# Performance work log

Measured on AMD Instinct MI355X. Metric: run time of the kernel, lower is better.

Reference implementation:

```python
import jax, jax.numpy as jnp
import numpy as np

FMAP = 160        # feature-map side -> N = FMAP*FMAP anchors
STRIDE = 4.0      # anchor grid stride in pixels
ANCHOR_SIZE = 32.0
NUM_CLASSES = 8
MAX_GT = 50
BATCH = 32


def setup_inputs() -> dict:
    key = jax.random.key(0)
    k0, k1, k2, k3, k4, k5 = jax.random.split(key, 6)
    B, C, H = BATCH, NUM_CLASSES, FMAP
    cls_output = jax.random.normal(k0, (B, C, 1, H, H), jnp.float32)
    reg_output = jax.random.normal(k1, (B, 4, 1, H, H), jnp.float32) * 0.3
    # anchor grid: one ANCHOR_SIZE box per feature-map cell; flatten order
    # matches torch's reshape over (H, W)
    c = (jnp.arange(H, dtype=jnp.float32) + 0.5) * STRIDE
    cy, cx = jnp.meshgrid(c, c, indexing='ij')   # row-major [H, W]
    cx = cx.reshape(-1); cy = cy.reshape(-1)
    half = ANCHOR_SIZE / 2.0
    anchors = jnp.stack([cx - half, cy - half, cx + half, cy + half], axis=1)
    # padded GT boxes, all geometrically valid (x1<x2, y1<y2)
    cxy = jax.random.uniform(k2, (B, MAX_GT, 2), jnp.float32, 64.0, 576.0)
    wh = jax.random.uniform(k3, (B, MAX_GT, 2), jnp.float32, 16.0, 128.0)
    gt_boxes = jnp.concatenate([cxy - wh / 2.0, cxy + wh / 2.0], axis=-1)
    gt_labels = jax.random.randint(k4, (B, MAX_GT), 0, NUM_CLASSES)
    num_boxes = jax.random.randint(k5, (B,), 0, MAX_GT + 1)
    return dict(cls_output=cls_output, reg_output=reg_output, anchors=anchors,
                gt_boxes=gt_boxes, gt_labels=gt_labels, num_boxes=num_boxes)


def _decode_boxes(reg, anchors):
    # inverse of the encoding in the loss: tx=(gt_cx-a_cx)*(4/aw) then (tx+1)/2
    aw = anchors[:, 2] - anchors[:, 0]
    ah = anchors[:, 3] - anchors[:, 1]
    acx = anchors[:, 0] + 0.5 * aw
    acy = anchors[:, 1] + 0.5 * ah
    tx = reg[..., 0] * 2.0 - 1.0
    ty = reg[..., 1] * 2.0 - 1.0
    cx = acx + tx * aw / 4.0
    cy = acy + ty * ah / 4.0
    w = aw * jnp.exp(reg[..., 2])
    h = ah * jnp.exp(reg[..., 3])
    return jnp.stack([cx - w / 2, cy - h / 2, cx + w / 2, cy + h / 2], axis=-1)


def _pairwise_iou(b1, b2):
    # b1 [B,N,4], b2 [B,M,4] -> [B,N,M]
    lt = jnp.maximum(b1[:, :, None, :2], b2[:, None, :, :2])
    rb = jnp.minimum(b1[:, :, None, 2:], b2[:, None, :, 2:])
    wh = jnp.clip(rb - lt, 0.0)
    inter = wh[..., 0] * wh[..., 1]
    a1 = (b1[..., 2] - b1[..., 0]) * (b1[..., 3] - b1[..., 1])
    a2 = (b2[..., 2] - b2[..., 0]) * (b2[..., 3] - b2[..., 1])
    return inter / jnp.maximum(a1[:, :, None] + a2[:, None, :] - inter, 1e-8)


def _smooth_l1(x):
    ax = jnp.abs(x)
    return jnp.where(ax < 1.0, 0.5 * x * x, ax - 0.5)


def _forward(cls_output, reg_output, anchors, gt_boxes, gt_labels, num_boxes):
    B, C = cls_output.shape[0], cls_output.shape[1]
    M = gt_boxes.shape[1]
    cls_i = cls_output.reshape(B, C, -1).transpose(0, 2, 1)   # [B,N,C]
    reg_i = reg_output.reshape(B, 4, -1).transpose(0, 2, 1)   # [B,N,4]
    decoded = _decode_boxes(reg_i, anchors)                    # [B,N,4]
    ious = _pairwise_iou(decoded, gt_boxes)                    # [B,N,M]
    valid = jnp.arange(M)[None, :] < num_boxes[:, None]        # [B,M]
    ious = jnp.where(valid[:, None, :], ious, -1.0)
    max_ious = ious.max(axis=-1)                               # [B,N]
    max_idx = ious.argmax(axis=-1)                             # [B,N]
    has = num_boxes > 0                                        # [B]
    pos = (max_ious >= 0.25) & has[:, None]
    neg = (max_ious < 0.1) & has[:, None]
    # classification
    logp = jax.nn.log_softmax(cls_i, axis=-1)
    tgt = jnp.take_along_axis(gt_labels, max_idx, axis=1)      # [B,N]
    ce_tgt = -jnp.take_along_axis(logp, tgt[..., None], axis=-1)[..., 0]
    ce_bg = -logp[..., 0]
    posf = pos.astype(cls_i.dtype)
    negf = neg.astype(cls_i.dtype)
    npos = posf.sum(-1)
    nneg = negf.sum(-1)
    cls_pos = jnp.where(npos > 0, (ce_tgt * posf).sum(-1) / jnp.maximum(npos, 1.0), 0.0)
    cls_neg = jnp.where(nneg > 0, (ce_bg * negf).sum(-1) / jnp.maximum(nneg, 1.0), 0.0)
    cls_losses = jnp.where(has, cls_pos + cls_neg, ce_bg.mean(-1))
    pg = jnp.take_along_axis(gt_boxes, max_idx[..., None], axis=1)  # [B,N,4]
    aw = anchors[:, 2] - anchors[:, 0]
    ah = anchors[:, 3] - anchors[:, 1]
    acx = anchors[:, 0] + 0.5 * aw
    acy = anchors[:, 1] + 0.5 * ah
    gw = pg[..., 2] - pg[..., 0]
    gh = pg[..., 3] - pg[..., 1]
    gcx = pg[..., 0] + 0.5 * gw
    gcy = pg[..., 1] + 0.5 * gh
    tx = ((gcx - acx) * (4.0 / aw) + 1.0) / 2.0
    ty = ((gcy - acy) * (4.0 / ah) + 1.0) / 2.0
    tw = jnp.log(jnp.maximum(gw, 1e-6) / aw)
    th = jnp.log(jnp.maximum(gh, 1e-6) / ah)
    reg_t = jnp.stack([tx, ty, tw, th], axis=-1)               # [B,N,4]
    sl = _smooth_l1(reg_i - reg_t)
    reg_losses = jnp.where(npos > 0,
                           (sl * posf[..., None]).sum((-1, -2)) / jnp.maximum(npos * 4.0, 1.0),
                           0.0)
    total_pos = npos.sum()
    cls_final = cls_losses.mean()
    reg_final = reg_losses.sum() / jnp.maximum(total_pos, 1.0)
    return cls_final + reg_final, cls_final, reg_final, total_pos


def reference(cls_output, reg_output, anchors, gt_boxes, gt_labels, num_boxes):
    return _forward(cls_output, reg_output, anchors, gt_boxes, gt_labels, num_boxes)
```

## Files before the change

kernel.cpp:

```cpp
#include <hip/hip_runtime.h>

#define FMAP 160
#define NANCH (FMAP * FMAP)
#define NCLS 8
#define MAXGT 50
#define BATCH 32
#define NT 256
#define TILES_X 5
#define TILES_Y 10
#define BLOCKS_PER_B (TILES_X * TILES_Y)
#define PSTRIDE 8

__device__ __forceinline__ float fc2(const float2& v, int k) {
    return k == 0 ? v.x : v.y;
}
__device__ __forceinline__ float sl1(float x) {
    float ax = fabsf(x);
    return ax < 1.f ? 0.5f * x * x : ax - 0.5f;
}

__global__ __launch_bounds__(NT) void detloss_main(
    const float* __restrict__ cls, const float* __restrict__ reg,
    const float* __restrict__ gtb, const int* __restrict__ gtl,
    const int* __restrict__ nb, float* __restrict__ partials)
{
    const int b  = blockIdx.y;
    const int t  = threadIdx.x;
    const int bx = blockIdx.x;
    const int tx = bx % TILES_X, ty = bx / TILES_X;
    const int w  = t >> 6, l = t & 63;
    const int R  = ty * 16 + w * 4 + (l >> 4);
    const int C  = tx * 16 + (l & 15);
    const int vt = R * (FMAP / 2) + C;

    const float2* regv = (const float2*)(reg + (size_t)b * 4 * NANCH);
    float2 rx = regv[0 * (NANCH / 2) + vt];
    float2 ry = regv[1 * (NANCH / 2) + vt];
    float2 rw = regv[2 * (NANCH / 2) + vt];
    float2 rh = regv[3 * (NANCH / 2) + vt];
    const float2* clsv = (const float2*)(cls + (size_t)b * NCLS * NANCH);
    float2 L[NCLS];
#pragma unroll
    for (int c = 0; c < NCLS; c++) L[c] = clsv[c * (NANCH / 2) + vt];

    __shared__ float4 gbox[64];
    __shared__ float  garea[64];
    __shared__ int    glab[64];
    if (t < MAXGT) {
        float4 g = ((const float4*)gtb)[b * MAXGT + t];
        gbox[t]  = g;
        garea[t] = (g.z - g.x) * (g.w - g.y);
        glab[t]  = gtl[b * MAXGT + t];
    }
    const int num = nb[b];

    const float acx0 = (float)((C * 2) * 4 + 2);
    const float acy  = (float)(R * 4 + 2);

    float x0[2], y0[2], x1[2], y1[2], a1[2];
#pragma unroll
    for (int k = 0; k < 2; k++) {
        float acx = acx0 + 4.f * (float)k;
        float txr = fc2(rx, k) * 2.f - 1.f;
        float tyr = fc2(ry, k) * 2.f - 1.f;
        float cx = acx + txr * 8.f;
        float cy = acy + tyr * 8.f;
        float ww = 32.f * __expf(fc2(rw, k));
        float hh = 32.f * __expf(fc2(rh, k));
        x0[k] = cx - 0.5f * ww; y0[k] = cy - 0.5f * hh;
        x1[k] = cx + 0.5f * ww; y1[k] = cy + 0.5f * hh;
        a1[k] = ww * hh;
    }

    float lse[2], cebg[2];
#pragma unroll
    for (int k = 0; k < 2; k++) {
        float s = 0.f;
#pragma unroll
        for (int c = 0; c < NCLS; c++) s += __expf(fc2(L[c], k));
        lse[k]  = __logf(s);
        cebg[k] = lse[k] - fc2(L[0], k);
    }

    float bx0 = fminf(x0[0], x0[1]);
    float by0 = fminf(y0[0], y0[1]);
    float bx1 = fmaxf(x1[0], x1[1]);
    float by1 = fmaxf(y1[0], y1[1]);
#pragma unroll
    for (int o = 1; o < 64; o <<= 1) {
        bx0 = fminf(bx0, __shfl_xor(bx0, o, 64));
        by0 = fminf(by0, __shfl_xor(by0, o, 64));
        bx1 = fmaxf(bx1, __shfl_xor(bx1, o, 64));
        by1 = fmaxf(by1, __shfl_xor(by1, o, 64));
    }

    __syncthreads();

    float4 gme = gbox[l];
    bool pass = (l < num) && (gme.x <= bx1) && (gme.z >= bx0)
                          && (gme.y <= by1) && (gme.w >= by0);
    unsigned long long mask = __ballot(pass);

    float bi[2] = {-1.f, -1.f};
    float bu[2] = { 1.f,  1.f};
    int   bidx[2] = {0, 0};
    while (mask) {
        int m = (int)__builtin_ctzll(mask);
        mask &= mask - 1;
        float4 g  = gbox[m];
        float  ga = garea[m];
#pragma unroll
        for (int k = 0; k < 2; k++) {
            float ltx = fmaxf(x0[k], g.x), lty = fmaxf(y0[k], g.y);
            float rbx = fminf(x1[k], g.z), rby = fminf(y1[k], g.w);
            float wx = fmaxf(rbx - ltx, 0.f), wy = fmaxf(rby - lty, 0.f);
            float inter = wx * wy;
            float u = a1[k] + ga - inter;
            bool better = inter * bu[k] > bi[k] * u;
            bi[k]   = better ? inter : bi[k];
            bu[k]   = better ? u     : bu[k];
            bidx[k] = better ? m     : bidx[k];
        }
    }

    float s_pk = 0.f, s_cp = 0.f, s_cn = 0.f, s_bg = 0.f, s_sl = 0.f;
    const bool has = num > 0;
#pragma unroll
    for (int k = 0; k < 2; k++) {
        s_bg += cebg[k];
        bool pos = has && (bi[k] >= 0.25f * bu[k]);
        bool neg = has && (bi[k] < 0.1f * bu[k]);
        s_pk += pos ? 1.f : (neg ? 4096.f : 0.f);
        s_cn += neg ? cebg[k] : 0.f;
        if (pos) {
            int tg = glab[bidx[k]];
            float e0 = (tg & 1) ? fc2(L[1], k) : fc2(L[0], k);
            float e1 = (tg & 1) ? fc2(L[3], k) : fc2(L[2], k);
            float e2 = (tg & 1) ? fc2(L[5], k) : fc2(L[4], k);
            float e3 = (tg & 1) ? fc2(L[7], k) : fc2(L[6], k);
            float f0 = (tg & 2) ? e1 : e0;
            float f1 = (tg & 2) ? e3 : e2;
            float ltg = (tg & 4) ? f1 : f0;
            s_cp += lse[k] - ltg;
            float4 gp = gbox[bidx[k]];
            float gw = gp.z - gp.x, gh = gp.w - gp.y;
            float gcx = gp.x + 0.5f * gw, gcy = gp.y + 0.5f * gh;
            float acx = acx0 + 4.f * (float)k;
            float txt = ((gcx - acx) * 0.125f + 1.f) * 0.5f;
            float tyt = ((gcy - acy) * 0.125f + 1.f) * 0.5f;
            float twt = __logf(fmaxf(gw, 1e-6f) * 0.03125f);
            float tht = __logf(fmaxf(gh, 1e-6f) * 0.03125f);
            s_sl += sl1(fc2(rx, k) - txt) + sl1(fc2(ry, k) - tyt)
                  + sl1(fc2(rw, k) - twt) + sl1(fc2(rh, k) - tht);
        }
    }

#pragma unroll
    for (int o = 32; o > 0; o >>= 1) {
        s_pk += __shfl_down(s_pk, o, 64);
        s_cp += __shfl_down(s_cp, o, 64);
        s_cn += __shfl_down(s_cn, o, 64);
        s_bg += __shfl_down(s_bg, o, 64);
        s_sl += __shfl_down(s_sl, o, 64);
    }
    __shared__ float red[4][5];
    if (l == 0) {
        red[w][0] = s_pk; red[w][1] = s_cp; red[w][2] = s_cn;
        red[w][3] = s_bg; red[w][4] = s_sl;
    }
    __syncthreads();
    if (t == 0) {
        float* p = partials + (size_t)(b * BLOCKS_PER_B + bx) * PSTRIDE;
        float4 v = make_float4(red[0][0] + red[1][0] + red[2][0] + red[3][0],
                               red[0][1] + red[1][1] + red[2][1] + red[3][1],
                               red[0][2] + red[1][2] + red[2][2] + red[3][2],
                               red[0][3] + red[1][3] + red[2][3] + red[3][3]);
        *(float4*)p = v;
        p[4] = red[0][4] + red[1][4] + red[2][4] + red[3][4];
    }
}

__global__ __launch_bounds__(NT) void detloss_final(
    const float* __restrict__ partials, const int* __restrict__ nb,
    float* __restrict__ out)
{
    const int t = threadIdx.x;
    const int img = t >> 3, sub = t & 7;
    float np = 0.f, nn = 0.f, cp = 0.f, cn = 0.f, bg = 0.f, sl = 0.f;
#pragma unroll
    for (int j = 0; j < 7; ++j) {
        int blk = sub + (j << 3);
        if (blk < BLOCKS_PER_B) {
            const float* p = partials + (size_t)(img * BLOCKS_PER_B + blk) * PSTRIDE;
            float pk  = p[0];
            float nnv = floorf(pk * (1.f / 4096.f));
            np += pk - 4096.f * nnv;
            nn += nnv;
            cp += p[1]; cn += p[2]; bg += p[3]; sl += p[4];
        }
    }
#pragma unroll
    for (int o = 4; o > 0; o >>= 1) {
        np += __shfl_down(np, o, 8);
        nn += __shfl_down(nn, o, 8);
        cp += __shfl_down(cp, o, 8);
        cn += __shfl_down(cn, o, 8);
        bg += __shfl_down(bg, o, 8);
        sl += __shfl_down(sl, o, 8);
    }
    __shared__ float acc[32][4];
    if (sub == 0) {
        bool hasb = nb[img] > 0;
        float clsb;
        if (hasb) {
            float a = (np > 0.f) ? cp / fmaxf(np, 1.f) : 0.f;
            float c = (nn > 0.f) ? cn / fmaxf(nn, 1.f) : 0.f;
            clsb = a + c;
        } else {
            clsb = bg / (float)NANCH;
        }
        float regb = (np > 0.f) ? sl / fmaxf(np * 4.f, 1.f) : 0.f;
        acc[img][0] = clsb; acc[img][1] = regb; acc[img][2] = np;
    }
    __syncthreads();
    if (t < 64) {
        float c = 0.f, r = 0.f, tp = 0.f;
        if (t < 32) { c = acc[t][0]; r = acc[t][1]; tp = acc[t][2]; }
#pragma unroll
        for (int o = 32; o > 0; o >>= 1) {
            c  += __shfl_down(c,  o, 64);
            r  += __shfl_down(r,  o, 64);
            tp += __shfl_down(tp, o, 64);
        }
        if (t == 0) {
            float clsf = c / (float)BATCH;
            float regf = r / fmaxf(tp, 1.f);
            out[0] = clsf + regf;
            out[1] = clsf;
            out[2] = regf;
            out[3] = tp;
        }
    }
}

extern "C" void kernel_launch(void* const* d_in, const int* in_sizes, int n_in,
                              void* d_out, int out_size, void* d_ws, size_t ws_size,
                              hipStream_t stream) {
    const float* cls = (const float*)d_in[0];
    const float* reg = (const float*)d_in[1];
    const float* gtb = (const float*)d_in[3];
    const int*   gtl = (const int*)d_in[4];
    const int*   nb  = (const int*)d_in[5];
    float* out      = (float*)d_out;
    float* partials = (float*)d_ws;

    dim3 grid(BLOCKS_PER_B, BATCH);
    detloss_main<<<grid, NT, 0, stream>>>(cls, reg, gtb, gtl, nb, partials);
    detloss_final<<<1, NT, 0, stream>>>(partials, nb, out);
}
```

Before: 18.45 us.

## Map one anchor per thread with 512-thread blocks instead of two

The main kernel switches from two anchors per thread (float2 loads) to one anchor per thread (scalar loads) and doubles the block to 512 threads. Each block still covers the same 32x16 anchor tile. Every wave now spans a narrower 32x2 region, so its bounding box is tighter and it should find fewer candidate GT boxes per IoU loop. Per-thread work halves and more waves expose parallelism, at the cost of narrower loads and twice as many waves doing the reductions.

Result: slower. 20.76 us (+12.5%).

```diff
diff --git a/kernel.cpp b/kernel.cpp
--- a/kernel.cpp
+++ b/kernel.cpp
@@ -5,15 +5,12 @@
 #define NCLS 8
 #define MAXGT 50
 #define BATCH 32
-#define NT 256
+#define NT 512
 #define TILES_X 5
 #define TILES_Y 10
 #define BLOCKS_PER_B (TILES_X * TILES_Y)
 #define PSTRIDE 8
 
-__device__ __forceinline__ float fc2(const float2& v, int k) {
-    return k == 0 ? v.x : v.y;
-}
 __device__ __forceinline__ float sl1(float x) {
     float ax = fabsf(x);
     return ax < 1.f ? 0.5f * x * x : ax - 0.5f;
@@ -29,19 +26,19 @@
     const int bx = blockIdx.x;
     const int tx = bx % TILES_X, ty = bx / TILES_X;
     const int w  = t >> 6, l = t & 63;
-    const int R  = ty * 16 + w * 4 + (l >> 4);
-    const int C  = tx * 16 + (l & 15);
-    const int vt = R * (FMAP / 2) + C;
-
-    const float2* regv = (const float2*)(reg + (size_t)b * 4 * NANCH);
-    float2 rx = regv[0 * (NANCH / 2) + vt];
-    float2 ry = regv[1 * (NANCH / 2) + vt];
-    float2 rw = regv[2 * (NANCH / 2) + vt];
-    float2 rh = regv[3 * (NANCH / 2) + vt];
-    const float2* clsv = (const float2*)(cls + (size_t)b * NCLS * NANCH);
-    float2 L[NCLS];
-#pragma unroll
-    for (int c = 0; c < NCLS; c++) L[c] = clsv[c * (NANCH / 2) + vt];
+    const int R  = ty * 16 + w * 2 + (l >> 5);
+    const int C  = tx * 32 + (l & 31);
+    const int n  = R * FMAP + C;
+
+    const float* regb_ = reg + (size_t)b * 4 * NANCH + n;
+    float rx = regb_[0];
+    float ry = regb_[1 * NANCH];
+    float rw = regb_[2 * NANCH];
+    float rh = regb_[3 * NANCH];
+    const float* clsb_ = cls + (size_t)b * NCLS * NANCH + n;
+    float L[NCLS];
+#pragma unroll
+    for (int c = 0; c < NCLS; c++) L[c] = clsb_[c * NANCH];
 
     __shared__ float4 gbox[64];
     __shared__ float  garea[64];
@@ -54,38 +51,26 @@
     }
     const int num = nb[b];
 
-    const float acx0 = (float)((C * 2) * 4 + 2);
-    const float acy  = (float)(R * 4 + 2);
-
-    float x0[2], y0[2], x1[2], y1[2], a1[2];
-#pragma unroll
-    for (int k = 0; k < 2; k++) {
-        float acx = acx0 + 4.f * (float)k;
-        float txr = fc2(rx, k) * 2.f - 1.f;
-        float tyr = fc2(ry, k) * 2.f - 1.f;
-        float cx = acx + txr * 8.f;
-        float cy = acy + tyr * 8.f;
-        float ww = 32.f * __expf(fc2(rw, k));
-        float hh = 32.f * __expf(fc2(rh, k));
-        x0[k] = cx - 0.5f * ww; y0[k] = cy - 0.5f * hh;
-        x1[k] = cx + 0.5f * ww; y1[k] = cy + 0.5f * hh;
-        a1[k] = ww * hh;
-    }
-
-    float lse[2], cebg[2];
-#pragma unroll
-    for (int k = 0; k < 2; k++) {
-        float s = 0.f;
-#pragma unroll
-        for (int c = 0; c < NCLS; c++) s += __expf(fc2(L[c], k));
-        lse[k]  = __logf(s);
-        cebg[k] = lse[k] - fc2(L[0], k);
-    }
-
-    float bx0 = fminf(x0[0], x0[1]);
-    float by0 = fminf(y0[0], y0[1]);
-    float bx1 = fmaxf(x1[0], x1[1]);
-    float by1 = fmaxf(y1[0], y1[1]);
+    const float acx = (float)(C * 4 + 2);
+    const float acy = (float)(R * 4 + 2);
+
+    float txr = rx * 2.f - 1.f;
+    float tyr = ry * 2.f - 1.f;
+    float cx = acx + txr * 8.f;
+    float cy = acy + tyr * 8.f;
+    float ww = 32.f * __expf(rw);
+    float hh = 32.f * __expf(rh);
+    float x0 = cx - 0.5f * ww, y0 = cy - 0.5f * hh;
+    float x1 = cx + 0.5f * ww, y1 = cy + 0.5f * hh;
+    float a1 = ww * hh;
+
+    float s = 0.f;
+#pragma unroll
+    for (int c = 0; c < NCLS; c++) s += __expf(L[c]);
+    float lse  = __logf(s);
+    float cebg = lse - L[0];
+
+    float bx0 = x0, by0 = y0, bx1 = x1, by1 = y1;
 #pragma unroll
     for (int o = 1; o < 64; o <<= 1) {
         bx0 = fminf(bx0, __shfl_xor(bx0, o, 64));
@@ -101,58 +86,48 @@
                           && (gme.y <= by1) && (gme.w >= by0);
     unsigned long long mask = __ballot(pass);
 
-    float bi[2] = {-1.f, -1.f};
-    float bu[2] = { 1.f,  1.f};
-    int   bidx[2] = {0, 0};
+    float bi = -1.f, bu = 1.f;
+    int   bidx = 0;
     while (mask) {
         int m = (int)__builtin_ctzll(mask);
         mask &= mask - 1;
         float4 g  = gbox[m];
         float  ga = garea[m];
-#pragma unroll
-        for (int k = 0; k < 2; k++) {
-            float ltx = fmaxf(x0[k], g.x), lty = fmaxf(y0[k], g.y);
-            float rbx = fminf(x1[k], g.z), rby = fminf(y1[k], g.w);
-            float wx = fmaxf(rbx - ltx, 0.f), wy = fmaxf(rby - lty, 0.f);
-            float inter = wx * wy;
-            float u = a1[k] + ga - inter;
-            bool better = inter * bu[k] > bi[k] * u;
-            bi[k]   = better ? inter : bi[k];
-            bu[k]   = better ? u     : bu[k];
-            bidx[k] = better ? m     : bidx[k];
-        }
-    }
-
-    float s_pk = 0.f, s_cp = 0.f, s_cn = 0.f, s_bg = 0.f, s_sl = 0.f;
+        float ltx = fmaxf(x0, g.x), lty = fmaxf(y0, g.y);
+        float rbx = fminf(x1, g.z), rby = fminf(y1, g.w);
+        float wx = fmaxf(rbx - ltx, 0.f), wy = fmaxf(rby - lty, 0.f);
+        float inter = wx * wy;
+        float u = a1 + ga - inter;
+        bool better = inter * bu > bi * u;
+        bi   = better ? inter : bi;
+        bu   = better ? u     : bu;
+        bidx = better ? m     : bidx;
+    }
+
+    float s_pk = 0.f, s_cp = 0.f, s_cn = 0.f, s_bg = cebg, s_sl = 0.f;
     const bool has = num > 0;
-#pragma unroll
-    for (int k = 0; k < 2; k++) {
-        s_bg += cebg[k];
-        bool pos = has && (bi[k] >= 0.25f * bu[k]);
-        bool neg = has && (bi[k] < 0.1f * bu[k]);
-        s_pk += pos ? 1.f : (neg ? 4096.f : 0.f);
-        s_cn += neg ? cebg[k] : 0.f;
-        if (pos) {
-            int tg = glab[bidx[k]];
-            float e0 = (tg & 1) ? fc2(L[1], k) : fc2(L[0], k);
-            float e1 = (tg & 1) ? fc2(L[3], k) : fc2(L[2], k);
-            float e2 = (tg & 1) ? fc2(L[5], k) : fc2(L[4], k);
-            float e3 = (tg & 1) ? fc2(L[7], k) : fc2(L[6], k);
-            float f0 = (tg & 2) ? e1 : e0;
-            float f1 = (tg & 2) ? e3 : e2;
-            float ltg = (tg & 4) ? f1 : f0;
-            s_cp += lse[k] - ltg;
-            float4 gp = gbox[bidx[k]];
-            float gw = gp.z - gp.x, gh = gp.w - gp.y;
-            float gcx = gp.x + 0.5f * gw, gcy = gp.y + 0.5f * gh;
-            float acx = acx0 + 4.f * (float)k;
-            float txt = ((gcx - acx) * 0.125f + 1.f) * 0.5f;
-            float tyt = ((gcy - acy) * 0.125f + 1.f) * 0.5f;
-            float twt = __logf(fmaxf(gw, 1e-6f) * 0.03125f);
-            float tht = __logf(fmaxf(gh, 1e-6f) * 0.03125f);
-            s_sl += sl1(fc2(rx, k) - txt) + sl1(fc2(ry, k) - tyt)
-                  + sl1(fc2(rw, k) - twt) + sl1(fc2(rh, k) - tht);
-        }
+    bool pos = has && (bi >= 0.25f * bu);
+    bool neg = has && (bi < 0.1f * bu);
+    s_pk = pos ? 1.f : (neg ? 4096.f : 0.f);
+    s_cn = neg ? cebg : 0.f;
+    if (pos) {
+        int tg = glab[bidx];
+        float e0 = (tg & 1) ? L[1] : L[0];
+        float e1 = (tg & 1) ? L[3] : L[2];
+        float e2 = (tg & 1) ? L[5] : L[4];
+        float e3 = (tg & 1) ? L[7] : L[6];
+        float f0 = (tg & 2) ? e1 : e0;
+        float f1 = (tg & 2) ? e3 : e2;
+        float ltg = (tg & 4) ? f1 : f0;
+        s_cp = lse - ltg;
+        float4 gp = gbox[bidx];
+        float gw = gp.z - gp.x, gh = gp.w - gp.y;
+        float gcx = gp.x + 0.5f * gw, gcy = gp.y + 0.5f * gh;
+        float txt = ((gcx - acx) * 0.125f + 1.f) * 0.5f;
+        float tyt = ((gcy - acy) * 0.125f + 1.f) * 0.5f;
+        float twt = __logf(fmaxf(gw, 1e-6f) * 0.03125f);
+        float tht = __logf(fmaxf(gh, 1e-6f) * 0.03125f);
+        s_sl = sl1(rx - txt) + sl1(ry - tyt) + sl1(rw - twt) + sl1(rh - tht);
     }
 
 #pragma unroll
@@ -163,24 +138,26 @@
         s_bg += __shfl_down(s_bg, o, 64);
         s_sl += __shfl_down(s_sl, o, 64);
     }
-    __shared__ float red[4][5];
+    __shared__ float red[8][5];
     if (l == 0) {
         red[w][0] = s_pk; red[w][1] = s_cp; red[w][2] = s_cn;
         red[w][3] = s_bg; red[w][4] = s_sl;
     }
     __syncthreads();
     if (t == 0) {
+        float a0 = 0.f, a1r = 0.f, a2 = 0.f, a3 = 0.f, a4 = 0.f;
+#pragma unroll
+        for (int j = 0; j < 8; j++) {
+            a0 += red[j][0]; a1r += red[j][1]; a2 += red[j][2];
+            a3 += red[j][3]; a4 += red[j][4];
+        }
         float* p = partials + (size_t)(b * BLOCKS_PER_B + bx) * PSTRIDE;
-        float4 v = make_float4(red[0][0] + red[1][0] + red[2][0] + red[3][0],
-                               red[0][1] + red[1][1] + red[2][1] + red[3][1],
-                               red[0][2] + red[1][2] + red[2][2] + red[3][2],
-                               red[0][3] + red[1][3] + red[2][3] + red[3][3]);
-        *(float4*)p = v;
-        p[4] = red[0][4] + red[1][4] + red[2][4] + red[3][4];
-    }
-}
-
-__global__ __launch_bounds__(NT) void detloss_final(
+        *(float4*)p = make_float4(a0, a1r, a2, a3);
+        p[4] = a4;
+    }
+}
+
+__global__ __launch_bounds__(256) void detloss_final(
     const float* __restrict__ partials, const int* __restrict__ nb,
     float* __restrict__ out)
 {
@@ -256,5 +233,5 @@
 
     dim3 grid(BLOCKS_PER_B, BATCH);
     detloss_main<<<grid, NT, 0, stream>>>(cls, reg, gtb, gtl, nb, partials);
-    detloss_final<<<1, NT, 0, stream>>>(partials, nb, out);
-}
+    detloss_final<<<1, 256, 0, stream>>>(partials, nb, out);
+}
```
